# Kernel optimization log

Hardware: AMD Instinct MI355X
Metric: run time of the kernel (lower is better)

The kernel has to match this reference:

```python
import jax, jax.numpy as jnp
import numpy as np

N = 100000
E = 1600000
IN_DIM, H1, H2, C = 256, 128, 128, 32


def setup_inputs() -> dict:
    key = jax.random.key(0)
    ks = jax.random.split(key, 8)
    X = jax.random.normal(ks[0], (N, IN_DIM), dtype=jnp.float32)
    edge_index = jax.random.randint(ks[1], (2, E), 0, N, dtype=jnp.int64)
    def glorot(k, shape):
        fan_in, fan_out = shape[0], shape[1]
        lim = (6.0 / (fan_in + fan_out)) ** 0.5
        return jax.random.uniform(k, shape, jnp.float32, -lim, lim)
    W1 = glorot(ks[2], (IN_DIM, H1))
    b1 = jnp.zeros((H1,), jnp.float32)
    W2 = glorot(ks[3], (H1, H2))
    b2 = jnp.zeros((H2,), jnp.float32)
    Wc = glorot(ks[4], (H2, C))
    bc = jnp.zeros((C,), jnp.float32)
    return {"X": X, "edge_index": edge_index, "W1": W1, "b1": b1,
            "W2": W2, "b2": b2, "Wc": Wc, "bc": bc}


def gcn_conv(x, src, dst, dinv, W, b, n):
    # PyG GCNConv: transform, then sym-normalized scatter-add with self-loops
    x = x @ W  # [N, out]
    norm = dinv[src] * dinv[dst]  # [E+N]
    msgs = x[src] * norm[:, None]  # [E+N, out] gather along edges
    out = jax.ops.segment_sum(msgs, dst, num_segments=n)
    return out + b


def reference(X, edge_index, W1, b1, W2, b2, Wc, bc):
    n = X.shape[0]
    loop = jnp.arange(n, dtype=edge_index.dtype)
    src = jnp.concatenate([edge_index[0], loop])
    dst = jnp.concatenate([edge_index[1], loop])
    # degree (with self-loops) at destination nodes
    deg = jax.ops.segment_sum(jnp.ones_like(dst, jnp.float32), dst, num_segments=n)
    dinv = jnp.where(deg > 0, jax.lax.rsqrt(deg), 0.0)
    h = jax.nn.relu(gcn_conv(X, src, dst, dinv, W1, b1, n))
    h = jax.nn.relu(gcn_conv(h, src, dst, dinv, W2, b2, n))
    logits = h @ Wc + bc
    return logits
```

## Files before the change

kernel.cpp:

```cpp
#include <hip/hip_runtime.h>
#include <hip/hip_bf16.h>
#include <hip/hip_fp16.h>

#define IN_DIM 256
#define HDIM 128
#define CDIM 32
#define NSUB 512
#define CHUNK 1024

typedef __attribute__((ext_vector_type(8))) unsigned short u16x8;
typedef __attribute__((ext_vector_type(8))) _Float16 f16x8;
typedef __attribute__((ext_vector_type(4))) float f32x4;
typedef __attribute__((ext_vector_type(4))) int int4v;

__device__ __forceinline__ int swz4(int r) { return (r & 3) ^ ((r >> 2) & 3); }


__global__ void zero512_kernel(int* __restrict__ p) {
    p[blockIdx.x * 256 + threadIdx.x] = 0;
}

__global__ __launch_bounds__(256) void hist512_kernel(const int* __restrict__ dst,
                                                      int* __restrict__ cnt512, int e, int nsr) {
    __shared__ int h[NSUB];
    for (int j = threadIdx.x; j < NSUB; j += 256) h[j] = 0;
    __syncthreads();
    const int stride = gridDim.x * 256;
    for (int i = blockIdx.x * 256 + threadIdx.x; i < e; i += stride) {
        int d = __builtin_nontemporal_load(&dst[i]);
        atomicAdd(&h[(unsigned)d / (unsigned)nsr], 1);
    }
    __syncthreads();
    for (int j = threadIdx.x; j < NSUB; j += 256)
        if (h[j]) atomicAdd(&cnt512[j], h[j]);
}

__global__ __launch_bounds__(256) void scan512_kernel(const int* __restrict__ cnt512,
                                                      int* __restrict__ rp512,
                                                      int* __restrict__ rcur512,
                                                      int* __restrict__ rcur8, int e) {
    __shared__ int sd[256];
    int t = threadIdx.x;
    int v0 = cnt512[2 * t], v1 = cnt512[2 * t + 1];
    sd[t] = v0 + v1;
    __syncthreads();
    for (int off = 1; off < 256; off <<= 1) {
        int x = (t >= off) ? sd[t - off] : 0;
        __syncthreads();
        sd[t] += x;
        __syncthreads();
    }
    int excl = sd[t] - (v0 + v1);
    rp512[2 * t] = excl;       rcur512[2 * t] = excl;
    rp512[2 * t + 1] = excl + v0; rcur512[2 * t + 1] = excl + v0;
    if (t == 255) rp512[512] = e;
    __syncthreads();
    if (t < 8) rcur8[t] = rp512[t * 64];
}

__global__ __launch_bounds__(256) void part8_kernel(
        const int* __restrict__ src, const int* __restrict__ dst,
        int* __restrict__ rcur8, long long* __restrict__ parts8, int e, int nsr) {
    __shared__ int cnt[8], base[8], cnt2[8];
    const int t = threadIdx.x;
    const int nchunk = (e + CHUNK - 1) / CHUNK;
    for (int c = blockIdx.x; c < nchunk; c += gridDim.x) {
        const int b0 = c * CHUNK;
        int s[4], d[4], r[4];
        if (t < 8) { cnt[t] = 0; cnt2[t] = 0; }
        __syncthreads();
        if (b0 + CHUNK <= e) {
            int4v sv = __builtin_nontemporal_load((const int4v*)(src + b0) + t);
            int4v dv = __builtin_nontemporal_load((const int4v*)(dst + b0) + t);
            s[0] = sv.x; s[1] = sv.y; s[2] = sv.z; s[3] = sv.w;
            d[0] = dv.x; d[1] = dv.y; d[2] = dv.z; d[3] = dv.w;
#pragma unroll
            for (int j = 0; j < 4; ++j) {
                r[j] = (int)((unsigned)d[j] / (unsigned)nsr) >> 6;
                atomicAdd(&cnt[r[j]], 1);
            }
        } else {
#pragma unroll
            for (int j = 0; j < 4; ++j) {
                int i = b0 + t * 4 + j;
                if (i < e) {
                    s[j] = src[i]; d[j] = dst[i];
                    r[j] = (int)((unsigned)d[j] / (unsigned)nsr) >> 6;
                    atomicAdd(&cnt[r[j]], 1);
                } else r[j] = -1;
            }
        }
        __syncthreads();
        if (t < 8) base[t] = cnt[t] ? atomicAdd(&rcur8[t], cnt[t]) : 0;
        __syncthreads();
#pragma unroll
        for (int j = 0; j < 4; ++j) {
            if (r[j] >= 0) {
                int off = atomicAdd(&cnt2[r[j]], 1);
                long long v = ((long long)(unsigned)d[j] << 32) | (unsigned)s[j];
                parts8[base[r[j]] + off] = v;
            }
        }
        __syncthreads();
    }
}

__global__ __launch_bounds__(256) void part64_kernel(
        const long long* __restrict__ parts8, const int* __restrict__ rp512,
        int* __restrict__ rcur512, long long* __restrict__ parts, int nsr) {
    __shared__ int cnt[64], base[64], cnt2[64];
    const int t = threadIdx.x;
    const int grp = blockIdx.x & 7;
    const int i0 = rp512[grp * 64];
    const int iE = rp512[grp * 64 + 64];
    const int nbg = gridDim.x >> 3;
    const int bi = blockIdx.x >> 3;
    const int nch = (iE - i0 + CHUNK - 1) / CHUNK;
    for (int c = bi; c < nch; c += nbg) {
        const int b0 = i0 + c * CHUNK;
        long long vv[4]; int r[4];
        if (t < 64) { cnt[t] = 0; cnt2[t] = 0; }
        __syncthreads();
#pragma unroll
        for (int j = 0; j < 4; ++j) {
            int i = b0 + t * 4 + j;
            if (i < iE) {
                vv[j] = parts8[i];
                int d = (int)(vv[j] >> 32);
                r[j] = (int)((unsigned)d / (unsigned)nsr) - grp * 64;
                atomicAdd(&cnt[r[j]], 1);
            } else r[j] = -1;
        }
        __syncthreads();
        if (t < 64) base[t] = cnt[t] ? atomicAdd(&rcur512[grp * 64 + t], cnt[t]) : 0;
        __syncthreads();
#pragma unroll
        for (int j = 0; j < 4; ++j) {
            if (r[j] >= 0) {
                int off = atomicAdd(&cnt2[r[j]], 1);
                parts[base[r[j]] + off] = vv[j];
            }
        }
        __syncthreads();
    }
}

__global__ __launch_bounds__(256) void sortplace_kernel(
        const long long* __restrict__ parts, const int* __restrict__ rp512,
        int* __restrict__ row_ptr, int* __restrict__ csr_src, float* __restrict__ dinv,
        int n, int nsr) {
    __shared__ int hist[256], sd[256], cur[256];
    const int b = blockIdx.x;
    const int d0 = b * nsr;
    if (d0 > n) return;
    const int i0 = rp512[b], iE = rp512[b + 1];
    const int t = threadIdx.x;
    hist[t] = 0;
    __syncthreads();
    for (int i = i0 + t; i < iE; i += 256) {
        int d = (int)(parts[i] >> 32);
        atomicAdd(&hist[d - d0], 1);
    }
    __syncthreads();
    int v = hist[t];
    sd[t] = v;
    __syncthreads();
    for (int off = 1; off < 256; off <<= 1) {
        int x = (t >= off) ? sd[t - off] : 0;
        __syncthreads();
        sd[t] += x;
        __syncthreads();
    }
    int excl = sd[t] - v;
    int node = d0 + t;
    if (t <= nsr && node <= n) row_ptr[node] = i0 + excl;
    if (t < nsr && node < n) dinv[node] = rsqrtf((float)(v + 1));
    cur[t] = i0 + excl;
    __syncthreads();
    for (int i = i0 + t; i < iE; i += 256) {
        long long vv = parts[i];
        int d = (int)(vv >> 32);
        int pos = atomicAdd(&cur[d - d0], 1);
        csr_src[pos] = (int)(vv & 0xffffffffLL);
    }
}


__global__ void wconv_kernel(const float* __restrict__ W, unsigned short* __restrict__ Wt,
                             int K, int N) {
    int i = blockIdx.x * blockDim.x + threadIdx.x;
    if (i < K * N) {
        int k = i / N, n2 = i % N;
        Wt[n2 * K + k] = __half_as_ushort(__float2half_rn(W[i]));
    }
}


template<int BN, bool AF16, bool BIAS, bool OUTH>
__global__ __launch_bounds__(256) void gemm_f16_kernel(
        const void* __restrict__ Ap, const unsigned short* __restrict__ Wt,
        const float* __restrict__ bias, void* __restrict__ C, int M, int K) {
    constexpr int FM = 4;
    constexpr int FN = BN / 2 / 16;
    constexpr int BU = (BN * 4 + 255) / 256;
    __shared__ __align__(16) unsigned short As[2][128 * 32];
    __shared__ __align__(16) unsigned short Bs[2][BN * 32];

    const int t = threadIdx.x;
    const int rowBase = blockIdx.x * 128;
    const int l = t & 63, w = t >> 6;
    const int wr = w >> 1, wc = w & 1;
    const int lrow = l & 15, g = l >> 4;
    const int NK = K >> 5;

    f32x4 acc[FM][FN];
#pragma unroll
    for (int i = 0; i < FM; ++i)
#pragma unroll
        for (int j = 0; j < FN; ++j) acc[i][j] = f32x4{0.f, 0.f, 0.f, 0.f};

    u16x8 aS[2];
    float4 af[2][2];
    u16x8 bS[BU];

    auto LOADA = [&](int k0) {
#pragma unroll
        for (int i = 0; i < 2; ++i) {
            int u = t + 256 * i;
            int r = u >> 2, c = u & 3;
            int gr = rowBase + r; if (gr > M - 1) gr = M - 1;
            if (AF16) {
                aS[i] = ((const u16x8*)((const unsigned short*)Ap + (size_t)gr * K + k0))[c];
            } else {
                const float4* ar = (const float4*)((const float*)Ap + (size_t)gr * K + k0);
                af[i][0] = ar[c * 2];
                af[i][1] = ar[c * 2 + 1];
            }
        }
    };
    auto WRITEA = [&](int buf) {
#pragma unroll
        for (int i = 0; i < 2; ++i) {
            int u = t + 256 * i;
            int r = u >> 2, c = u & 3;
            int d = r * 4 + (c ^ swz4(r));
            if (AF16) {
                ((u16x8*)As[buf])[d] = aS[i];
            } else {
                f16x8 h;
                h[0] = (_Float16)af[i][0].x; h[1] = (_Float16)af[i][0].y;
                h[2] = (_Float16)af[i][0].z; h[3] = (_Float16)af[i][0].w;
                h[4] = (_Float16)af[i][1].x; h[5] = (_Float16)af[i][1].y;
                h[6] = (_Float16)af[i][1].z; h[7] = (_Float16)af[i][1].w;
                ((f16x8*)As[buf])[d] = h;
            }
        }
    };
    auto LOADB = [&](int k0) {
#pragma unroll
        for (int i = 0; i < BU; ++i) {
            int u = t + 256 * i;
            if (u < BN * 4) {
                int nn = u >> 2, c = u & 3;
                bS[i] = ((const u16x8*)(Wt + (size_t)nn * K + k0))[c];
            }
        }
    };
    auto WRITEB = [&](int buf) {
#pragma unroll
        for (int i = 0; i < BU; ++i) {
            int u = t + 256 * i;
            if (u < BN * 4) {
                int nn = u >> 2, c = u & 3;
                ((u16x8*)Bs[buf])[nn * 4 + (c ^ swz4(nn))] = bS[i];
            }
        }
    };

    LOADA(0); LOADB(0);
    WRITEA(0); WRITEB(0);
    __syncthreads();

    for (int k = 0; k < NK; ++k) {
        int cur = k & 1;
        bool more = (k + 1 < NK);
        if (more) { LOADA((k + 1) << 5); LOADB((k + 1) << 5); }

        f16x8 a[FM], b[FN];
#pragma unroll
        for (int fm = 0; fm < FM; ++fm) {
            int r = wr * 64 + fm * 16 + lrow;
            a[fm] = ((const f16x8*)As[cur])[r * 4 + (g ^ swz4(r))];
        }
#pragma unroll
        for (int fn = 0; fn < FN; ++fn) {
            int nn = wc * (FN * 16) + fn * 16 + lrow;
            b[fn] = ((const f16x8*)Bs[cur])[nn * 4 + (g ^ swz4(nn))];
        }
#pragma unroll
        for (int fm = 0; fm < FM; ++fm)
#pragma unroll
            for (int fn = 0; fn < FN; ++fn)
                acc[fm][fn] = __builtin_amdgcn_mfma_f32_16x16x32_f16(a[fm], b[fn], acc[fm][fn], 0, 0, 0);

        if (more) { WRITEA(cur ^ 1); WRITEB(cur ^ 1); }
        __syncthreads();
    }

#pragma unroll
    for (int fm = 0; fm < FM; ++fm)
#pragma unroll
        for (int fn = 0; fn < FN; ++fn) {
            int col = wc * (FN * 16) + fn * 16 + lrow;
#pragma unroll
            for (int r = 0; r < 4; ++r) {
                int row = rowBase + wr * 64 + fm * 16 + g * 4 + r;
                if (row < M) {
                    float v = acc[fm][fn][r];
                    if (BIAS) v += bias[col];
                    if (OUTH) ((__half*)C)[(size_t)row * BN + col] = __float2half_rn(v);
                    else      ((float*)C)[(size_t)row * BN + col] = v;
                }
            }
        }
}


__global__ __launch_bounds__(256) void gather_kernel(
        const __half* __restrict__ x, const int* __restrict__ row_ptr,
        const int* __restrict__ csr_src, const float* __restrict__ dinv,
        const float* __restrict__ bias, __half* __restrict__ out, int n) {
    int node = __builtin_amdgcn_readfirstlane(blockIdx.x * 4 + (threadIdx.x >> 6));
    if (node >= n) return;
    int lane = threadIdx.x & 63;
    const __half2* xv = (const __half2*)x;
    float dd = dinv[node];
    float2 self = __half22float2(xv[(size_t)node * 64 + lane]);
    float accx = dd * self.x, accy = dd * self.y;
    int p = row_ptr[node], end = row_ptr[node + 1];
    for (; p + 3 < end; p += 4) {
        int s0 = csr_src[p], s1 = csr_src[p + 1], s2 = csr_src[p + 2], s3 = csr_src[p + 3];
        float w0 = dinv[s0], w1 = dinv[s1], w2 = dinv[s2], w3 = dinv[s3];
        float2 v0 = __half22float2(xv[(size_t)s0 * 64 + lane]);
        float2 v1 = __half22float2(xv[(size_t)s1 * 64 + lane]);
        float2 v2 = __half22float2(xv[(size_t)s2 * 64 + lane]);
        float2 v3 = __half22float2(xv[(size_t)s3 * 64 + lane]);
        accx += w0 * v0.x + w1 * v1.x + w2 * v2.x + w3 * v3.x;
        accy += w0 * v0.y + w1 * v1.y + w2 * v2.y + w3 * v3.y;
    }
    for (; p < end; ++p) {
        int s0 = csr_src[p];
        float w0 = dinv[s0];
        float2 v0 = __half22float2(xv[(size_t)s0 * 64 + lane]);
        accx += w0 * v0.x;
        accy += w0 * v0.y;
    }
    float2 bb = ((const float2*)bias)[lane];
    float2 r;
    r.x = fmaxf(accx * dd + bb.x, 0.f);
    r.y = fmaxf(accy * dd + bb.y, 0.f);
    ((__half2*)out)[(size_t)node * 64 + lane] = __float22half2_rn(r);
}


extern "C" void kernel_launch(void* const* d_in, const int* in_sizes, int n_in,
                              void* d_out, int out_size, void* d_ws, size_t ws_size,
                              hipStream_t stream) {
    const float* X  = (const float*)d_in[0];
    const int*   ei = (const int*)d_in[1];
    const float* W1 = (const float*)d_in[2];
    const float* b1 = (const float*)d_in[3];
    const float* W2 = (const float*)d_in[4];
    const float* b2 = (const float*)d_in[5];
    const float* Wc = (const float*)d_in[6];
    const float* bc = (const float*)d_in[7];
    float* out = (float*)d_out;

    const int n = in_sizes[0] / IN_DIM;
    const int e = in_sizes[1] / 2;
    const int* src = ei;
    const int* dst = ei + e;
    const int nsr = (n + NSUB - 1) / NSUB;

    char* ws = (char*)d_ws;
    auto align = [](size_t x) { return (x + 255) & ~(size_t)255; };
    size_t off = 0;
    float* dinv   = (float*)(ws + off); off += align((size_t)n * 4);
    int* row_ptr  = (int*)(ws + off);   off += align((size_t)(n + 1) * 4);
    int* cnt512   = (int*)(ws + off);   off += align(512 * 4);
    int* rp512    = (int*)(ws + off);   off += align(513 * 4);
    int* rcur512  = (int*)(ws + off);   off += align(512 * 4);
    int* rcur8    = (int*)(ws + off);   off += align(8 * 4);
    long long* parts8 = (long long*)(ws + off); off += align((size_t)e * 8);
    long long* parts  = (long long*)(ws + off); off += align((size_t)e * 8);
    unsigned short* w1t = (unsigned short*)(ws + off); off += align((size_t)IN_DIM * HDIM * 2);
    unsigned short* w2t = (unsigned short*)(ws + off); off += align((size_t)HDIM * HDIM * 2);
    unsigned short* wct = (unsigned short*)(ws + off); off += align((size_t)HDIM * CDIM * 2);
    __half* bufAh = (__half*)(ws + off); off += align((size_t)n * HDIM * 2);
    __half* bufBh = (__half*)(ws + off); off += align((size_t)n * HDIM * 2);
    int* csr_src  = (int*)parts8;

    wconv_kernel<<<(IN_DIM * HDIM + 255) / 256, 256, 0, stream>>>(W1, w1t, IN_DIM, HDIM);
    wconv_kernel<<<(HDIM * HDIM + 255) / 256, 256, 0, stream>>>(W2, w2t, HDIM, HDIM);
    wconv_kernel<<<(HDIM * CDIM + 255) / 256, 256, 0, stream>>>(Wc, wct, HDIM, CDIM);

    zero512_kernel<<<2, 256, 0, stream>>>(cnt512);
    hist512_kernel<<<256, 256, 0, stream>>>(dst, cnt512, e, nsr);
    scan512_kernel<<<1, 256, 0, stream>>>(cnt512, rp512, rcur512, rcur8, e);
    part8_kernel<<<1024, 256, 0, stream>>>(src, dst, rcur8, parts8, e, nsr);
    part64_kernel<<<1024, 256, 0, stream>>>(parts8, rp512, rcur512, parts, nsr);
    sortplace_kernel<<<NSUB, 256, 0, stream>>>(parts, rp512, row_ptr, csr_src, dinv, n, nsr);

    const int gBlocks = (n + 127) / 128;
    const int nb_g = (n + 3) / 4;

    gemm_f16_kernel<128, false, false, true><<<gBlocks, 256, 0, stream>>>(X, w1t, nullptr, bufAh, n, IN_DIM);
    gather_kernel<<<nb_g, 256, 0, stream>>>(bufAh, row_ptr, csr_src, dinv, b1, bufBh, n);

    gemm_f16_kernel<128, true, false, true><<<gBlocks, 256, 0, stream>>>(bufBh, w2t, nullptr, bufAh, n, HDIM);
    gather_kernel<<<nb_g, 256, 0, stream>>>(bufAh, row_ptr, csr_src, dinv, b2, bufBh, n);

    gemm_f16_kernel<32, true, true, false><<<gBlocks, 256, 0, stream>>>(bufBh, wct, bc, out, n, HDIM);
}
```

Before: 272.4 us.

## Fuse second aggregation with classifier GEMM, unroll gather by 8, merge weight converts

Fuses the layer-2 neighbor aggregation with the final 128x32 classifier matmul. Each block aggregates 16 nodes into LDS and one wave applies MFMA plus bias, so the layer-2 hidden activations are no longer written to and re-read from global memory, and one launch goes away. The gather loops also get an 8-wide unrolled path to keep more independent loads in flight, and the three weight-conversion launches become one. The trade-off is that only one of four waves does the classifier work, and the extra unrolling raises register pressure.

```diff
diff --git a/kernel.cpp b/kernel.cpp
--- a/kernel.cpp
+++ b/kernel.cpp
@@ -186,12 +186,23 @@
 }
 
 
-__global__ void wconv_kernel(const float* __restrict__ W, unsigned short* __restrict__ Wt,
-                             int K, int N) {
-    int i = blockIdx.x * blockDim.x + threadIdx.x;
-    if (i < K * N) {
-        int k = i / N, n2 = i % N;
-        Wt[n2 * K + k] = __half_as_ushort(__float2half_rn(W[i]));
+__global__ void wconv_all_kernel(const float* __restrict__ W1, const float* __restrict__ W2,
+                                 const float* __restrict__ Wc,
+                                 unsigned short* __restrict__ w1t, unsigned short* __restrict__ w2t,
+                                 unsigned short* __restrict__ wct) {
+    int i = blockIdx.x * 256 + threadIdx.x;
+    const int s1 = IN_DIM * HDIM;
+    const int s2 = s1 + HDIM * HDIM;
+    const int s3 = s2 + HDIM * CDIM;
+    if (i < s1) {
+        int k = i / HDIM, n2 = i % HDIM;
+        w1t[n2 * IN_DIM + k] = __half_as_ushort(__float2half_rn(W1[i]));
+    } else if (i < s2) {
+        int j = i - s1; int k = j / HDIM, n2 = j % HDIM;
+        w2t[n2 * HDIM + k] = __half_as_ushort(__float2half_rn(W2[j]));
+    } else if (i < s3) {
+        int j = i - s2; int k = j / CDIM, n2 = j % CDIM;
+        wct[n2 * HDIM + k] = __half_as_ushort(__float2half_rn(Wc[j]));
     }
 }
 
@@ -338,6 +349,17 @@
     float2 self = __half22float2(xv[(size_t)node * 64 + lane]);
     float accx = dd * self.x, accy = dd * self.y;
     int p = row_ptr[node], end = row_ptr[node + 1];
+    for (; p + 7 < end; p += 8) {
+        int s[8]; float w[8]; float2 v[8];
+#pragma unroll
+        for (int j = 0; j < 8; ++j) s[j] = csr_src[p + j];
+#pragma unroll
+        for (int j = 0; j < 8; ++j) w[j] = dinv[s[j]];
+#pragma unroll
+        for (int j = 0; j < 8; ++j) v[j] = __half22float2(xv[(size_t)s[j] * 64 + lane]);
+#pragma unroll
+        for (int j = 0; j < 8; ++j) { accx += w[j] * v[j].x; accy += w[j] * v[j].y; }
+    }
     for (; p + 3 < end; p += 4) {
         int s0 = csr_src[p], s1 = csr_src[p + 1], s2 = csr_src[p + 2], s3 = csr_src[p + 3];
         float w0 = dinv[s0], w1 = dinv[s1], w2 = dinv[s2], w3 = dinv[s3];
@@ -360,6 +382,91 @@
     r.x = fmaxf(accx * dd + bb.x, 0.f);
     r.y = fmaxf(accy * dd + bb.y, 0.f);
     ((__half2*)out)[(size_t)node * 64 + lane] = __float22half2_rn(r);
+}
+
+
+__global__ __launch_bounds__(256) void gather_cls_kernel(
+        const __half* __restrict__ x, const int* __restrict__ row_ptr,
+        const int* __restrict__ csr_src, const float* __restrict__ dinv,
+        const float* __restrict__ b2, const unsigned short* __restrict__ wct,
+        const float* __restrict__ bc, float* __restrict__ out, int n) {
+    __shared__ __align__(16) __half h_lds[16][136];
+    const int w = threadIdx.x >> 6;
+    const int lane = threadIdx.x & 63;
+    const int node0 = blockIdx.x * 16;
+    const __half2* xv = (const __half2*)x;
+    const float2 bb = ((const float2*)b2)[lane];
+
+#pragma unroll
+    for (int j = 0; j < 4; ++j) {
+        int row = w * 4 + j;
+        int node = __builtin_amdgcn_readfirstlane(node0 + row);
+        float2 rv = make_float2(0.f, 0.f);
+        if (node < n) {
+            float dd = dinv[node];
+            float2 self = __half22float2(xv[(size_t)node * 64 + lane]);
+            float accx = dd * self.x, accy = dd * self.y;
+            int p = row_ptr[node], end = row_ptr[node + 1];
+            for (; p + 7 < end; p += 8) {
+                int s[8]; float wt[8]; float2 v[8];
+#pragma unroll
+                for (int q = 0; q < 8; ++q) s[q] = csr_src[p + q];
+#pragma unroll
+                for (int q = 0; q < 8; ++q) wt[q] = dinv[s[q]];
+#pragma unroll
+                for (int q = 0; q < 8; ++q) v[q] = __half22float2(xv[(size_t)s[q] * 64 + lane]);
+#pragma unroll
+                for (int q = 0; q < 8; ++q) { accx += wt[q] * v[q].x; accy += wt[q] * v[q].y; }
+            }
+            for (; p + 3 < end; p += 4) {
+                int s0 = csr_src[p], s1 = csr_src[p + 1], s2 = csr_src[p + 2], s3 = csr_src[p + 3];
+                float w0 = dinv[s0], w1 = dinv[s1], w2 = dinv[s2], w3 = dinv[s3];
+                float2 v0 = __half22float2(xv[(size_t)s0 * 64 + lane]);
+                float2 v1 = __half22float2(xv[(size_t)s1 * 64 + lane]);
+                float2 v2 = __half22float2(xv[(size_t)s2 * 64 + lane]);
+                float2 v3 = __half22float2(xv[(size_t)s3 * 64 + lane]);
+                accx += w0 * v0.x + w1 * v1.x + w2 * v2.x + w3 * v3.x;
+                accy += w0 * v0.y + w1 * v1.y + w2 * v2.y + w3 * v3.y;
+            }
+            for (; p < end; ++p) {
+                int s0 = csr_src[p];
+                float w0 = dinv[s0];
+                float2 v0 = __half22float2(xv[(size_t)s0 * 64 + lane]);
+                accx += w0 * v0.x;
+                accy += w0 * v0.y;
+            }
+            rv.x = fmaxf(accx * dd + bb.x, 0.f);
+            rv.y = fmaxf(accy * dd + bb.y, 0.f);
+        }
+        *(__half2*)&h_lds[row][2 * lane] = __float22half2_rn(rv);
+    }
+    __syncthreads();
+
+    if (w == 0) {
+        const int lrow = lane & 15, g = lane >> 4;
+        f32x4 acc[2];
+        acc[0] = f32x4{0.f, 0.f, 0.f, 0.f};
+        acc[1] = f32x4{0.f, 0.f, 0.f, 0.f};
+#pragma unroll
+        for (int k0 = 0; k0 < HDIM; k0 += 32) {
+            f16x8 a = *(const f16x8*)&h_lds[lrow][k0 + 8 * g];
+#pragma unroll
+            for (int fn = 0; fn < 2; ++fn) {
+                f16x8 b = *(const f16x8*)((const _Float16*)wct + (fn * 16 + lrow) * HDIM + k0 + 8 * g);
+                acc[fn] = __builtin_amdgcn_mfma_f32_16x16x32_f16(a, b, acc[fn], 0, 0, 0);
+            }
+        }
+#pragma unroll
+        for (int fn = 0; fn < 2; ++fn) {
+            int col = fn * 16 + lrow;
+            float bcv = bc[col];
+#pragma unroll
+            for (int r = 0; r < 4; ++r) {
+                int node = node0 + g * 4 + r;
+                if (node < n) out[(size_t)node * CDIM + col] = acc[fn][r] + bcv;
+            }
+        }
+    }
 }
 
 
@@ -400,9 +507,8 @@
     __half* bufBh = (__half*)(ws + off); off += align((size_t)n * HDIM * 2);
     int* csr_src  = (int*)parts8;
 
-    wconv_kernel<<<(IN_DIM * HDIM + 255) / 256, 256, 0, stream>>>(W1, w1t, IN_DIM, HDIM);
-    wconv_kernel<<<(HDIM * HDIM + 255) / 256, 256, 0, stream>>>(W2, w2t, HDIM, HDIM);
-    wconv_kernel<<<(HDIM * CDIM + 255) / 256, 256, 0, stream>>>(Wc, wct, HDIM, CDIM);
+    wconv_all_kernel<<<(IN_DIM * HDIM + HDIM * HDIM + HDIM * CDIM + 255) / 256, 256, 0, stream>>>(
+        W1, W2, Wc, w1t, w2t, wct);
 
     zero512_kernel<<<2, 256, 0, stream>>>(cnt512);
     hist512_kernel<<<256, 256, 0, stream>>>(dst, cnt512, e, nsr);
@@ -418,7 +524,6 @@
     gather_kernel<<<nb_g, 256, 0, stream>>>(bufAh, row_ptr, csr_src, dinv, b1, bufBh, n);
 
     gemm_f16_kernel<128, true, false, true><<<gBlocks, 256, 0, stream>>>(bufBh, w2t, nullptr, bufAh, n, HDIM);
-    gather_kernel<<<nb_g, 256, 0, stream>>>(bufAh, row_ptr, csr_src, dinv, b2, bufBh, n);
-
-    gemm_f16_kernel<32, true, true, false><<<gBlocks, 256, 0, stream>>>(bufBh, wct, bc, out, n, HDIM);
-}
+
+    gather_cls_kernel<<<(n + 15) / 16, 256, 0, stream>>>(bufAh, row_ptr, csr_src, dinv, b2, wct, bc, out, n);
+}
```

After: 254.9 us. 1.07x faster.
